# Performance work log

Measured on AMD Instinct MI355X. Metric: run time of the kernel, lower is better.

The kernel has to match this reference:

```python
import jax, jax.numpy as jnp
import numpy as np

B, L, V, OOV, E, H = 16, 256, 50000, 100, 128, 128
PAD_IDX, PLACEHOLDER_IDX = 0, 1


def lstm(x, W_ih, W_hh, b):
    # x: (B, T, I) -> hidden states (B, T, H); PyTorch gate order i,f,g,o
    nh = W_hh.shape[1]
    xg = jnp.einsum('bti,gi->btg', x, W_ih) + b  # precompute input gates

    def step(carry, xt):
        h, c = carry
        g = xt + h @ W_hh.T
        i, f, gg, o = jnp.split(g, 4, axis=-1)
        c = jax.nn.sigmoid(f) * c + jax.nn.sigmoid(i) * jnp.tanh(gg)
        h = jax.nn.sigmoid(o) * jnp.tanh(c)
        return (h, c), h

    bsz = x.shape[0]
    init = (jnp.zeros((bsz, nh), x.dtype), jnp.zeros((bsz, nh), x.dtype))
    _, hs = jax.lax.scan(step, init, jnp.swapaxes(xg, 0, 1))
    return jnp.swapaxes(hs, 0, 1)


def setup_inputs() -> dict:
    key = jax.random.key(0)
    ks = jax.random.split(key, 20)
    s = 0.05
    return {
        'src_tokens': jax.random.randint(ks[0], (B, L), 2, V),
        'src_lens': jnp.full((B,), L, dtype=jnp.int64 if jax.config.jax_enable_x64 else jnp.int32),
        'prev_output_tokens': jax.random.randint(ks[1], (B, 1), 2, V),
        'prev_output_lens': jnp.ones((B,), jnp.int32),
        'src_tokens_with_oov': jax.random.randint(ks[2], (B, L), 2, V + OOV),
        'oov_counts': jax.random.randint(ks[3], (B,), 0, OOV + 1),
        'decoder_state': jax.random.normal(ks[4], (B, H), jnp.float32),
        'embedding': jax.random.normal(ks[5], (V, E), jnp.float32) * 0.02,
        'enc_W_ih': jax.random.normal(ks[6], (4 * H, E), jnp.float32) * s,
        'enc_W_hh': jax.random.normal(ks[7], (4 * H, H), jnp.float32) * s,
        'enc_b': jnp.zeros((4 * H,), jnp.float32),
        'dec_W_ih': jax.random.normal(ks[8], (4 * H, E + H), jnp.float32) * s,
        'dec_W_hh': jax.random.normal(ks[9], (4 * H, H), jnp.float32) * s,
        'dec_b': jnp.zeros((4 * H,), jnp.float32),
        'attn_W': jax.random.normal(ks[10], (H, H), jnp.float32) * s,
        'out_W': jax.random.normal(ks[11], (H, 2 * H), jnp.float32) * s,
        'out_b': jnp.zeros((H,), jnp.float32),
        'copy_W': jax.random.normal(ks[12], (H, H), jnp.float32) * s,
        'gen_W': jax.random.normal(ks[13], (V + OOV, H), jnp.float32) * 0.02,
    }


def reference(src_tokens, src_lens, prev_output_tokens, prev_output_lens,
              src_tokens_with_oov, oov_counts, decoder_state,
              embedding, enc_W_ih, enc_W_hh, enc_b,
              dec_W_ih, dec_W_hh, dec_b,
              attn_W, out_W, out_b, copy_W, gen_W):
    neg_inf = -jnp.inf
    # ---- encoder ----
    enc_out = lstm(embedding[src_tokens], enc_W_ih, enc_W_hh, enc_b)  # B,L,H
    pad_mask = src_tokens == PAD_IDX                                   # B,L

    # ---- copy-state attention (selective read) ----
    mask = (prev_output_tokens == src_tokens).astype(enc_out.dtype)[..., None]  # B,L,1
    agg_w = jnp.tanh(jnp.einsum('blh,gh->blg', mask * enc_out, copy_W))
    cw = jax.nn.softmax(jnp.einsum('blg,bg->bl', agg_w, decoder_state), axis=1)
    copy_state = jnp.einsum('bl,blh->bh', cw, enc_out)

    # ---- decoder LSTM single step ----
    src_embed = embedding[prev_output_tokens[:, 0]]                    # B,E
    dec_in = jnp.concatenate([src_embed, copy_state], -1)[:, None, :]
    rnn_out = lstm(dec_in, dec_W_ih, dec_W_hh, dec_b)[:, 0]           # B,H

    # ---- attention ----
    scores = jnp.einsum('bh,blh->bl', rnn_out @ attn_W.T, enc_out)
    scores = jnp.where(pad_mask, neg_inf, scores)
    aw = jax.nn.softmax(scores, axis=1)
    ctx = jnp.einsum('bl,blh->bh', aw, enc_out)
    attn_out = jnp.tanh(jnp.concatenate([rnn_out, ctx], -1) @ out_W.T + out_b)

    # ---- generate + copy logits ----
    gen_logits = attn_out @ gen_W.T                                    # B,V+OOV
    b_idx = jnp.broadcast_to(jnp.arange(B)[:, None], (B, L))
    # scatter-reduce: equivalent to dense src_map (B, V+OOV, L) @ enc_out
    agg = jnp.zeros((B, V + OOV, H), enc_out.dtype).at[b_idx, src_tokens_with_oov].add(enc_out)
    copy_wts = jnp.tanh(jnp.einsum('bvh,gh->bvg', agg, copy_W))
    copy_score = jnp.einsum('bvg,bg->bv', copy_wts, attn_out)
    pos = jnp.arange(V + OOV)[None]
    copy_score = jnp.where(pos >= V + oov_counts[:, None], neg_inf, copy_score)

    total = gen_logits + copy_score
    total = jnp.where(pos == PLACEHOLDER_IDX, neg_inf, total)
    total_prob = jax.nn.softmax(total, axis=1)
    return total_prob, enc_out, attn_out
```

## Files before the change

kernel.cpp:

```cpp
#include <hip/hip_runtime.h>
#include <math.h>

#define B_   16
#define L_   256
#define V_   50000
#define NV_  50100
#define E_   128
#define H_   128
#define G4_  512
#define CHUNK_ 1566

typedef float f32x4 __attribute__((ext_vector_type(4)));
typedef float f32x2 __attribute__((ext_vector_type(2)));

__device__ __forceinline__ float sigm(float x){ return 1.0f/(1.0f+__expf(-x)); }
__device__ __forceinline__ float tanh_fast(float x){
  x = fminf(15.0f, fmaxf(-15.0f, x));
  float t = __expf(2.0f*x);
  return (t-1.0f)/(t+1.0f);
}

__global__ __launch_bounds__(512) void enc_xg_kernel(
    const int* __restrict__ tok, const float* __restrict__ emb,
    const float* __restrict__ Wih, const float* __restrict__ bias,
    float* __restrict__ xg)
{
  __shared__ __align__(16) float sx[8*128];
  int r0 = blockIdx.x*8;
  int t = threadIdx.x;
  for (int i=t; i<8*128; i+=512){
    int r=i>>7, e=i&127;
    sx[i] = emb[(size_t)tok[r0+r]*E_ + e];
  }
  __syncthreads();
  int g = t;
  float acc[8];
  #pragma unroll
  for (int r=0;r<8;r++) acc[r]=0.f;
  const float4* wr = (const float4*)(Wih + (size_t)g*E_);
  #pragma unroll 4
  for (int i=0;i<32;i++){
    float4 w = wr[i];
    #pragma unroll
    for (int r=0;r<8;r++){
      float4 x = ((const float4*)(sx + r*128))[i];
      acc[r] += w.x*x.x + w.y*x.y + w.z*x.z + w.w*x.w;
    }
  }
  float bg = bias[g];
  #pragma unroll
  for (int r=0;r<8;r++) xg[(size_t)(r0+r)*G4_ + g] = acc[r] + bg;
}

__global__ __launch_bounds__(512, 2) void enc_lstm_kernel(
    const float* __restrict__ xg, const float* __restrict__ Whh,
    float* __restrict__ enc_out)
{
  int b = blockIdx.x;
  int g = threadIdx.x;
  f32x2 w2[64];
  {
    const f32x4* wr4 = (const f32x4*)(Whh + (size_t)g*H_);
    #pragma unroll
    for (int k=0;k<32;k++){
      f32x4 wv = wr4[k];
      w2[2*k]   = wv.xy;
      w2[2*k+1] = wv.zw;
    }
  }

  __shared__ __align__(16) float sh_h[128];
  __shared__ float sh_g[512];
  if (g<128) sh_h[g]=0.f;
  float c = 0.f;
  const float* xgb = xg + (size_t)b*L_*G4_;
  float* eob = enc_out + (size_t)b*L_*H_;
  __syncthreads();

  const f32x4* sh4 = (const f32x4*)sh_h;
  bool is_gg = (g>=256 && g<384);
  float xcur = xgb[g];
  for (int t=0;t<L_;t++){
    float xnext = (t<L_-1) ? xgb[(t+1)*G4_ + g] : 0.f;
    f32x2 a0 = {xcur, 0.f}, a1 = {0.f,0.f}, a2 = {0.f,0.f}, a3 = {0.f,0.f};
    #pragma unroll
    for (int k=0;k<32;k+=4){
      f32x4 h0=sh4[k], h1=sh4[k+1], h2v=sh4[k+2], h3=sh4[k+3];
      a0 += w2[2*k+0]*h0.xy;  a1 += w2[2*k+1]*h0.zw;
      a2 += w2[2*k+2]*h1.xy;  a3 += w2[2*k+3]*h1.zw;
      a0 += w2[2*k+4]*h2v.xy; a1 += w2[2*k+5]*h2v.zw;
      a2 += w2[2*k+6]*h3.xy;  a3 += w2[2*k+7]*h3.zw;
    }
    f32x2 as = (a0+a1)+(a2+a3);
    float acc = as.x + as.y;
    float act = is_gg ? tanh_fast(acc) : sigm(acc);
    sh_g[g] = act;
    __syncthreads();
    if (g < 128){
      c = sh_g[128+g]*c + sh_g[g]*sh_g[256+g];
      float h = sh_g[384+g]*tanh_fast(c);
      sh_h[g] = h;
      eob[t*H_ + g] = h;
    }
    __syncthreads();
    xcur = xnext;
  }
}

__global__ __launch_bounds__(128) void copy_score1_kernel(
    const int* __restrict__ src, const int* __restrict__ prev,
    const float* __restrict__ enc_out, const float* __restrict__ cW,
    const float* __restrict__ dstate, float* __restrict__ s)
{
  int bl = blockIdx.x; int b = bl>>8;
  if (src[bl] != prev[b]){ if (threadIdx.x==0) s[bl]=0.f; return; }
  __shared__ __align__(16) float se[128];
  __shared__ float sred[2];
  int g = threadIdx.x;
  se[g] = enc_out[(size_t)bl*H_ + g];
  __syncthreads();
  const float4* wr = (const float4*)(cW + (size_t)g*H_);
  float acc=0.f;
  #pragma unroll
  for (int i=0;i<32;i++){
    float4 wv=wr[i]; float4 e=((const float4*)se)[i];
    acc += wv.x*e.x + wv.y*e.y + wv.z*e.z + wv.w*e.w;
  }
  float v = tanhf(acc)*dstate[b*H_+g];
  #pragma unroll
  for (int o=32;o;o>>=1) v += __shfl_down(v,o);
  if ((g&63)==0) sred[g>>6]=v;
  __syncthreads();
  if (g==0) s[bl]=sred[0]+sred[1];
}

__global__ __launch_bounds__(512) void fuse_mid_kernel(
    const float* __restrict__ scopy, const float* __restrict__ enc_out,
    const int* __restrict__ prev, const float* __restrict__ emb,
    const float* __restrict__ dWih, const float* __restrict__ db,
    const int* __restrict__ src, const float* __restrict__ aW,
    const float* __restrict__ oW, const float* __restrict__ ob,
    float* __restrict__ attn_out)
{
  int b=blockIdx.x, t=threadIdx.x;
  __shared__ float sw[256];
  __shared__ float spart[512];
  __shared__ float sred[4];
  __shared__ __align__(16) float sin_[256];
  __shared__ float sg[512];
  __shared__ __align__(16) float sr[128];
  __shared__ __align__(16) float sq[128];
  __shared__ float sc[256];
  __shared__ __align__(16) float sctx[128];

  float v = (t<256) ? scopy[b*L_+t] : -INFINITY;
  {
    float m=v;
    #pragma unroll
    for (int o=32;o;o>>=1) m=fmaxf(m,__shfl_down(m,o));
    if (t<256 && (t&63)==0) sred[t>>6]=m;
  }
  __syncthreads();
  float m4 = fmaxf(fmaxf(sred[0],sred[1]),fmaxf(sred[2],sred[3]));
  __syncthreads();
  float e = (t<256) ? __expf(v-m4) : 0.f;
  {
    float z=e;
    #pragma unroll
    for (int o=32;o;o>>=1) z += __shfl_down(z,o);
    if (t<256 && (t&63)==0) sred[t>>6]=z;
  }
  __syncthreads();
  {
    float z4 = sred[0]+sred[1]+sred[2]+sred[3];
    if (t<256) sw[t] = e/z4;
  }
  __syncthreads();

  {
    int ch=t>>7, h=t&127;
    float acc=0.f;
    const float* eb = enc_out + (size_t)b*L_*H_;
    for (int l=ch*64; l<ch*64+64; l++) acc += sw[l]*eb[(size_t)l*H_+h];
    spart[t]=acc;
  }
  __syncthreads();
  if (t<128){
    float cst = spart[t]+spart[128+t]+spart[256+t]+spart[384+t];
    sin_[128+t]=cst;
    sin_[t]=emb[(size_t)prev[b]*E_+t];
  }
  __syncthreads();

  {
    const f32x4* wr=(const f32x4*)(dWih + (size_t)t*256);
    const f32x4* x4=(const f32x4*)sin_;
    f32x2 d0={db[t],0.f}, d1={0.f,0.f}, d2={0.f,0.f}, d3={0.f,0.f};
    #pragma unroll
    for (int k=0;k<64;k+=4){
      f32x4 xa=x4[k], xb=x4[k+1], xc=x4[k+2], xd=x4[k+3];
      f32x4 wa=wr[k], wb=wr[k+1], wc=wr[k+2], wd=wr[k+3];
      d0 += wa.xy*xa.xy; d1 += wa.zw*xa.zw;
      d2 += wb.xy*xb.xy; d3 += wb.zw*xb.zw;
      d0 += wc.xy*xc.xy; d1 += wc.zw*xc.zw;
      d2 += wd.xy*xd.xy; d3 += wd.zw*xd.zw;
    }
    f32x2 dsm=(d0+d1)+(d2+d3);
    sg[t]=dsm.x+dsm.y;
  }
  __syncthreads();
  if (t<128){
    float iv=sg[t], gv=sg[256+t], ov=sg[384+t];
    float cc = sigm(iv)*tanhf(gv);
    sr[t] = sigm(ov)*tanhf(cc);
  }
  __syncthreads();

  if (t<128){
    const f32x4* wr=(const f32x4*)(aW + (size_t)t*H_);
    const f32x4* x4=(const f32x4*)sr;
    float acc=0.f;
    #pragma unroll
    for (int i=0;i<32;i++){
      f32x4 wv=wr[i], x=x4[i];
      acc += wv.x*x.x + wv.y*x.y + wv.z*x.z + wv.w*x.w;
    }
    sq[t]=acc;
  }
  __syncthreads();

  if (t<256){
    const f32x4* e4=(const f32x4*)(enc_out + ((size_t)b*L_+t)*H_);
    const f32x4* q4=(const f32x4*)sq;
    float acc=0.f;
    #pragma unroll
    for (int i=0;i<32;i++){
      f32x4 ev=e4[i], q=q4[i];
      acc += ev.x*q.x + ev.y*q.y + ev.z*q.z + ev.w*q.w;
    }
    if (src[b*L_+t]==0) acc=-INFINITY;
    sc[t]=acc;
  }
  __syncthreads();

  v = (t<256) ? sc[t] : -INFINITY;
  {
    float m=v;
    #pragma unroll
    for (int o=32;o;o>>=1) m=fmaxf(m,__shfl_down(m,o));
    if (t<256 && (t&63)==0) sred[t>>6]=m;
  }
  __syncthreads();
  m4 = fmaxf(fmaxf(sred[0],sred[1]),fmaxf(sred[2],sred[3]));
  __syncthreads();
  e = (t<256) ? __expf(v-m4) : 0.f;
  {
    float z=e;
    #pragma unroll
    for (int o=32;o;o>>=1) z += __shfl_down(z,o);
    if (t<256 && (t&63)==0) sred[t>>6]=z;
  }
  __syncthreads();
  {
    float z4 = sred[0]+sred[1]+sred[2]+sred[3];
    if (t<256) sc[t] = e/z4;
  }
  __syncthreads();

  {
    int ch=t>>7, h=t&127;
    float acc=0.f;
    const float* eb = enc_out + (size_t)b*L_*H_;
    for (int l=ch*64; l<ch*64+64; l++) acc += sc[l]*eb[(size_t)l*H_+h];
    spart[t]=acc;
  }
  __syncthreads();
  if (t<128) sctx[t] = spart[t]+spart[128+t]+spart[256+t]+spart[384+t];
  __syncthreads();

  if (t<128){
    const f32x4* wr=(const f32x4*)(oW + (size_t)t*256);
    const f32x4* r4=(const f32x4*)sr;
    const f32x4* c4=(const f32x4*)sctx;
    float acc=ob[t];
    #pragma unroll
    for (int i=0;i<32;i++){
      f32x4 wv=wr[i], x=r4[i];
      acc += wv.x*x.x + wv.y*x.y + wv.z*x.z + wv.w*x.w;
    }
    #pragma unroll
    for (int i=0;i<32;i++){
      f32x4 wv=wr[32+i], x=c4[i];
      acc += wv.x*x.x + wv.y*x.y + wv.z*x.z + wv.w*x.w;
    }
    attn_out[b*H_+t]=tanhf(acc);
  }
}

__global__ __launch_bounds__(256) void copy_agg_kernel(
    const int* __restrict__ stw, const float* __restrict__ enc_out,
    float* __restrict__ agg, int* __restrict__ replist, int* __restrict__ repcnt)
{
  int b=blockIdx.x, l=threadIdx.x;
  __shared__ int stok[256];
  __shared__ int scnt;
  stok[l] = stw[b*L_+l];
  if (l==0) scnt=0;
  __syncthreads();
  int tok = stok[l];
  int first=0;
  while (stok[first]!=tok) first++;
  if (first==l){
    int myidx = atomicAdd(&scnt,1);
    float4 acc[32];
    #pragma unroll
    for (int i=0;i<32;i++) acc[i]=make_float4(0.f,0.f,0.f,0.f);
    for (int l2=l; l2<L_; l2++){
      if (stok[l2]==tok){
        const float4* e=(const float4*)(enc_out + ((size_t)b*L_+l2)*H_);
        #pragma unroll
        for (int i=0;i<32;i++){
          float4 v=e[i];
          acc[i].x+=v.x; acc[i].y+=v.y; acc[i].z+=v.z; acc[i].w+=v.w;
        }
      }
    }
    float4* dst=(float4*)(agg + ((size_t)b*L_+l)*H_);
    #pragma unroll
    for (int i=0;i<32;i++) dst[i]=acc[i];
    replist[b*L_+myidx]=l;
  }
  __syncthreads();
  if (l==0) repcnt[b]=scnt;
}

__global__ __launch_bounds__(256) void gen_logits_kernel(
    const float* __restrict__ attn_out, const float* __restrict__ gW,
    const int* __restrict__ oovc, float* __restrict__ total)
{
  __shared__ float sa[B_*H_];
  __shared__ float sw[64*129];
  int t=threadIdx.x;
  int v0=blockIdx.x*64;
  for (int i=t;i<B_*H_;i+=256) sa[i]=attn_out[i];
  for (int i=t;i<64*32;i+=256){
    int r=i>>5, cc=i&31;
    if (v0+r<NV_){
      float4 wv = ((const float4*)(gW + (size_t)(v0+r)*H_))[cc];
      float* dst = sw + r*129 + cc*4;
      dst[0]=wv.x; dst[1]=wv.y; dst[2]=wv.z; dst[3]=wv.w;
    }
  }
  __syncthreads();
  int vl=t&63, bq=t>>6;
  int v=v0+vl;
  if (v>=NV_) return;
  float acc[4]={0.f,0.f,0.f,0.f};
  const float* wrow = sw + vl*129;
  #pragma unroll 8
  for (int h4=0; h4<32; h4++){
    float w0=wrow[h4*4+0], w1=wrow[h4*4+1], w2=wrow[h4*4+2], w3=wrow[h4*4+3];
    #pragma unroll
    for (int k=0;k<4;k++){
      float4 a = ((const float4*)(sa + (bq*4+k)*H_))[h4];
      acc[k] += w0*a.x + w1*a.y + w2*a.z + w3*a.w;
    }
  }
  #pragma unroll
  for (int k=0;k<4;k++){
    int b=bq*4+k;
    float o = (v==1 || v >= V_ + oovc[b]) ? -INFINITY : acc[k];
    total[(size_t)b*NV_ + v] = o;
  }
}

__global__ __launch_bounds__(128) void copy_score2_kernel(
    const int* __restrict__ stw, const float* __restrict__ agg,
    const float* __restrict__ cW, const float* __restrict__ attn_out,
    const int* __restrict__ replist, const int* __restrict__ repcnt,
    float* __restrict__ total)
{
  int b=blockIdx.x;
  int cnt=repcnt[b];
  int g=threadIdx.x;
  __shared__ __align__(16) float srow[128];
  __shared__ float sred[2];
  float aog = attn_out[b*H_+g];
  float4 w[32];
  const float4* wrow=(const float4*)(cW + (size_t)g*H_);
  #pragma unroll
  for (int i=0;i<32;i++) w[i]=wrow[i];
  for (int ri=blockIdx.y; ri<cnt; ri+=gridDim.y){
    int l = replist[b*L_+ri];
    srow[g] = agg[((size_t)b*L_+l)*H_+g];
    __syncthreads();
    float acc=0.f;
    #pragma unroll
    for (int i=0;i<32;i++){
      float4 e=((const float4*)srow)[i]; float4 wv=w[i];
      acc += wv.x*e.x + wv.y*e.y + wv.z*e.z + wv.w*e.w;
    }
    float v = tanhf(acc)*aog;
    #pragma unroll
    for (int o=32;o;o>>=1) v += __shfl_down(v,o);
    if ((g&63)==0) sred[g>>6]=v;
    __syncthreads();
    if (g==0){
      int vtok = stw[b*L_+l];
      total[(size_t)b*NV_ + vtok] += sred[0]+sred[1];
    }
    __syncthreads();
  }
}

__global__ __launch_bounds__(256) void vocab_pass1_kernel(
    const float* __restrict__ total, float* __restrict__ pmax, float* __restrict__ psum)
{
  int b=blockIdx.x, j=blockIdx.y, t=threadIdx.x;
  int lo=j*CHUNK_, hi=min(lo+CHUNK_, NV_);
  const float* row = total + (size_t)b*NV_;
  __shared__ float sred[4];
  float m=-INFINITY;
  for (int i=lo+t;i<hi;i+=256) m=fmaxf(m,row[i]);
  #pragma unroll
  for (int o=32;o;o>>=1) m=fmaxf(m,__shfl_down(m,o));
  if ((t&63)==0) sred[t>>6]=m;
  __syncthreads();
  m = fmaxf(fmaxf(sred[0],sred[1]),fmaxf(sred[2],sred[3]));
  __syncthreads();
  float s=0.f;
  if (m > -INFINITY){
    for (int i=lo+t;i<hi;i+=256) s += __expf(row[i]-m);
    #pragma unroll
    for (int o=32;o;o>>=1) s += __shfl_down(s,o);
  }
  if ((t&63)==0) sred[t>>6]=s;
  __syncthreads();
  if (t==0){ pmax[b*32+j]=m; psum[b*32+j]=sred[0]+sred[1]+sred[2]+sred[3]; }
}

__global__ void vocab_pass2_kernel(const float* __restrict__ pmax,
                                   const float* __restrict__ psum, float* __restrict__ MZ)
{
  int b=blockIdx.x, t=threadIdx.x;
  float mj = pmax[b*32+t];
  float m = mj;
  #pragma unroll
  for (int o=16;o;o>>=1) m=fmaxf(m,__shfl_down(m,o));
  m = __shfl(m,0);
  float z = psum[b*32+t]*__expf(mj-m);
  #pragma unroll
  for (int o=16;o;o>>=1) z += __shfl_down(z,o);
  if (t==0){ MZ[b]=m; MZ[16+b]=z; }
}

__global__ __launch_bounds__(256) void vocab_pass3_kernel(
    float* __restrict__ total, const float* __restrict__ MZ)
{
  int b=blockIdx.x, j=blockIdx.y, t=threadIdx.x;
  int lo=j*CHUNK_, hi=min(lo+CHUNK_, NV_);
  float m=MZ[b], rz=1.0f/MZ[16+b];
  float* row = total + (size_t)b*NV_;
  for (int i=lo+t;i<hi;i+=256) row[i] = __expf(row[i]-m)*rz;
}

extern "C" void kernel_launch(void* const* d_in, const int* in_sizes, int n_in,
                              void* d_out, int out_size, void* d_ws, size_t ws_size,
                              hipStream_t stream)
{
  const int*   src_tokens = (const int*)d_in[0];
  const int*   prev_tok   = (const int*)d_in[2];
  const int*   stw        = (const int*)d_in[4];
  const int*   oovc       = (const int*)d_in[5];
  const float* dstate     = (const float*)d_in[6];
  const float* emb        = (const float*)d_in[7];
  const float* enc_Wih    = (const float*)d_in[8];
  const float* enc_Whh    = (const float*)d_in[9];
  const float* enc_b      = (const float*)d_in[10];
  const float* dec_Wih    = (const float*)d_in[11];
  const float* dec_b      = (const float*)d_in[13];
  const float* attn_W     = (const float*)d_in[14];
  const float* out_W      = (const float*)d_in[15];
  const float* out_b      = (const float*)d_in[16];
  const float* copy_W     = (const float*)d_in[17];
  const float* gen_W      = (const float*)d_in[18];

  float* out      = (float*)d_out;
  float* total    = out;
  float* enc_out  = out + (size_t)B_*NV_;
  float* attn_out = enc_out + (size_t)B_*L_*H_;

  float* ws     = (float*)d_ws;
  float* xg     = ws;
  float* agg    = xg + (size_t)B_*L_*G4_;
  float* scopy  = agg + (size_t)B_*L_*H_;
  float* pmax   = scopy + B_*L_;
  float* psum   = pmax + 512;
  float* MZ     = psum + 512;
  int*   replist= (int*)(MZ + 32);
  int*   repcnt = replist + B_*L_;

  enc_xg_kernel<<<B_*L_/8, 512, 0, stream>>>(src_tokens, emb, enc_Wih, enc_b, xg);
  enc_lstm_kernel<<<B_, 512, 0, stream>>>(xg, enc_Whh, enc_out);
  copy_score1_kernel<<<B_*L_, 128, 0, stream>>>(src_tokens, prev_tok, enc_out, copy_W, dstate, scopy);
  copy_agg_kernel<<<B_, 256, 0, stream>>>(stw, enc_out, agg, replist, repcnt);
  fuse_mid_kernel<<<B_, 512, 0, stream>>>(scopy, enc_out, prev_tok, emb, dec_Wih, dec_b,
                                          src_tokens, attn_W, out_W, out_b, attn_out);
  gen_logits_kernel<<<(NV_+63)/64, 256, 0, stream>>>(attn_out, gen_W, oovc, total);
  copy_score2_kernel<<<dim3(B_,32), 128, 0, stream>>>(stw, agg, copy_W, attn_out, replist, repcnt, total);
  vocab_pass1_kernel<<<dim3(B_,32), 256, 0, stream>>>(total, pmax, psum);
  vocab_pass2_kernel<<<B_, 32, 0, stream>>>(pmax, psum, MZ);
  vocab_pass3_kernel<<<dim3(B_,32), 256, 0, stream>>>(total, MZ);
}
```

Baseline: 340.8 us.

## Fuse copy-score into mid kernel, merge vocab reductions, retile encoder input GEMM

```diff
diff --git a/kernel.cpp b/kernel.cpp
--- a/kernel.cpp
+++ b/kernel.cpp
@@ -25,34 +25,35 @@
     const float* __restrict__ Wih, const float* __restrict__ bias,
     float* __restrict__ xg)
 {
-  __shared__ __align__(16) float sx[8*128];
-  int r0 = blockIdx.x*8;
+  __shared__ __align__(16) float sx[16*128];
+  int r0 = blockIdx.x*16;
   int t = threadIdx.x;
-  for (int i=t; i<8*128; i+=512){
+  for (int i=t; i<16*128; i+=512){
     int r=i>>7, e=i&127;
     sx[i] = emb[(size_t)tok[r0+r]*E_ + e];
   }
   __syncthreads();
   int g = t;
-  float acc[8];
-  #pragma unroll
-  for (int r=0;r<8;r++) acc[r]=0.f;
-  const float4* wr = (const float4*)(Wih + (size_t)g*E_);
-  #pragma unroll 4
+  float acc[16];
+  #pragma unroll
+  for (int r=0;r<16;r++) acc[r]=0.f;
+  const f32x4* wr = (const f32x4*)(Wih + (size_t)g*E_);
+  #pragma unroll 2
   for (int i=0;i<32;i++){
-    float4 w = wr[i];
-    #pragma unroll
-    for (int r=0;r<8;r++){
-      float4 x = ((const float4*)(sx + r*128))[i];
+    f32x4 w = wr[i];
+    #pragma unroll
+    for (int r=0;r<16;r++){
+      f32x4 x = ((const f32x4*)(sx + r*128))[i];
       acc[r] += w.x*x.x + w.y*x.y + w.z*x.z + w.w*x.w;
     }
   }
   float bg = bias[g];
   #pragma unroll
-  for (int r=0;r<8;r++) xg[(size_t)(r0+r)*G4_ + g] = acc[r] + bg;
-}
-
-__global__ __launch_bounds__(512, 2) void enc_lstm_kernel(
+  for (int r=0;r<16;r++) xg[(size_t)(r0+r)*G4_ + g] = acc[r] + bg;
+}
+
+__global__ void __attribute__((amdgpu_flat_work_group_size(512,512), amdgpu_waves_per_eu(2,2)))
+enc_lstm_kernel(
     const float* __restrict__ xg, const float* __restrict__ Whh,
     float* __restrict__ enc_out)
 {
@@ -68,6 +69,8 @@
       w2[2*k+1] = wv.zw;
     }
   }
+  #pragma unroll
+  for (int k=0;k<64;k++) asm volatile("" : "+v"(w2[k]));
 
   __shared__ __align__(16) float sh_h[128];
   __shared__ float sh_g[512];
@@ -107,42 +110,19 @@
   }
 }
 
-__global__ __launch_bounds__(128) void copy_score1_kernel(
+__global__ __launch_bounds__(512) void fuse_mid_kernel(
     const int* __restrict__ src, const int* __restrict__ prev,
     const float* __restrict__ enc_out, const float* __restrict__ cW,
-    const float* __restrict__ dstate, float* __restrict__ s)
-{
-  int bl = blockIdx.x; int b = bl>>8;
-  if (src[bl] != prev[b]){ if (threadIdx.x==0) s[bl]=0.f; return; }
+    const float* __restrict__ dstate, const float* __restrict__ emb,
+    const float* __restrict__ dWih, const float* __restrict__ db,
+    const float* __restrict__ aW, const float* __restrict__ oW,
+    const float* __restrict__ ob, float* __restrict__ attn_out)
+{
+  int b=blockIdx.x, t=threadIdx.x;
+  __shared__ float s_scopy[256];
+  __shared__ int   mlist[256];
+  __shared__ int   mcnt;
   __shared__ __align__(16) float se[128];
-  __shared__ float sred[2];
-  int g = threadIdx.x;
-  se[g] = enc_out[(size_t)bl*H_ + g];
-  __syncthreads();
-  const float4* wr = (const float4*)(cW + (size_t)g*H_);
-  float acc=0.f;
-  #pragma unroll
-  for (int i=0;i<32;i++){
-    float4 wv=wr[i]; float4 e=((const float4*)se)[i];
-    acc += wv.x*e.x + wv.y*e.y + wv.z*e.z + wv.w*e.w;
-  }
-  float v = tanhf(acc)*dstate[b*H_+g];
-  #pragma unroll
-  for (int o=32;o;o>>=1) v += __shfl_down(v,o);
-  if ((g&63)==0) sred[g>>6]=v;
-  __syncthreads();
-  if (g==0) s[bl]=sred[0]+sred[1];
-}
-
-__global__ __launch_bounds__(512) void fuse_mid_kernel(
-    const float* __restrict__ scopy, const float* __restrict__ enc_out,
-    const int* __restrict__ prev, const float* __restrict__ emb,
-    const float* __restrict__ dWih, const float* __restrict__ db,
-    const int* __restrict__ src, const float* __restrict__ aW,
-    const float* __restrict__ oW, const float* __restrict__ ob,
-    float* __restrict__ attn_out)
-{
-  int b=blockIdx.x, t=threadIdx.x;
   __shared__ float sw[256];
   __shared__ float spart[512];
   __shared__ float sred[4];
@@ -153,7 +133,37 @@
   __shared__ float sc[256];
   __shared__ __align__(16) float sctx[128];
 
-  float v = (t<256) ? scopy[b*L_+t] : -INFINITY;
+  if (t==0) mcnt=0;
+  __syncthreads();
+  if (t<256){
+    s_scopy[t]=0.f;
+    if (src[b*L_+t]==prev[b]){ int i=atomicAdd(&mcnt,1); mlist[i]=t; }
+  }
+  __syncthreads();
+  for (int mi=0; mi<mcnt; mi++){
+    int l = mlist[mi];
+    if (t<128) se[t] = enc_out[((size_t)b*L_+l)*H_ + t];
+    __syncthreads();
+    if (t<128){
+      const f32x4* wr = (const f32x4*)(cW + (size_t)t*H_);
+      const f32x4* e4 = (const f32x4*)se;
+      float acc=0.f;
+      #pragma unroll
+      for (int i=0;i<32;i++){
+        f32x4 wv=wr[i], e=e4[i];
+        acc += wv.x*e.x + wv.y*e.y + wv.z*e.z + wv.w*e.w;
+      }
+      float v = tanhf(acc)*dstate[b*H_+t];
+      #pragma unroll
+      for (int o=32;o;o>>=1) v += __shfl_down(v,o);
+      if ((t&63)==0) sred[t>>6]=v;
+    }
+    __syncthreads();
+    if (t==0) s_scopy[l]=sred[0]+sred[1];
+    __syncthreads();
+  }
+
+  float v = (t<256) ? s_scopy[t] : -INFINITY;
   {
     float m=v;
     #pragma unroll
@@ -312,20 +322,17 @@
   while (stok[first]!=tok) first++;
   if (first==l){
     int myidx = atomicAdd(&scnt,1);
-    float4 acc[32];
-    #pragma unroll
-    for (int i=0;i<32;i++) acc[i]=make_float4(0.f,0.f,0.f,0.f);
+    f32x4 acc[32];
+    #pragma unroll
+    for (int i=0;i<32;i++) acc[i]=(f32x4){0.f,0.f,0.f,0.f};
     for (int l2=l; l2<L_; l2++){
       if (stok[l2]==tok){
-        const float4* e=(const float4*)(enc_out + ((size_t)b*L_+l2)*H_);
+        const f32x4* e=(const f32x4*)(enc_out + ((size_t)b*L_+l2)*H_);
         #pragma unroll
-        for (int i=0;i<32;i++){
-          float4 v=e[i];
-          acc[i].x+=v.x; acc[i].y+=v.y; acc[i].z+=v.z; acc[i].w+=v.w;
-        }
+        for (int i=0;i<32;i++) acc[i]+=e[i];
       }
     }
-    float4* dst=(float4*)(agg + ((size_t)b*L_+l)*H_);
+    f32x4* dst=(f32x4*)(agg + ((size_t)b*L_+l)*H_);
     #pragma unroll
     for (int i=0;i<32;i++) dst[i]=acc[i];
     replist[b*L_+myidx]=l;
@@ -386,8 +393,8 @@
   __shared__ __align__(16) float srow[128];
   __shared__ float sred[2];
   float aog = attn_out[b*H_+g];
-  float4 w[32];
-  const float4* wrow=(const float4*)(cW + (size_t)g*H_);
+  f32x4 w[32];
+  const f32x4* wrow=(const f32x4*)(cW + (size_t)g*H_);
   #pragma unroll
   for (int i=0;i<32;i++) w[i]=wrow[i];
   for (int ri=blockIdx.y; ri<cnt; ri+=gridDim.y){
@@ -397,7 +404,7 @@
     float acc=0.f;
     #pragma unroll
     for (int i=0;i<32;i++){
-      float4 e=((const float4*)srow)[i]; float4 wv=w[i];
+      f32x4 e=((const f32x4*)srow)[i]; f32x4 wv=w[i];
       acc += wv.x*e.x + wv.y*e.y + wv.z*e.z + wv.w*e.w;
     }
     float v = tanhf(acc)*aog;
@@ -413,48 +420,42 @@
   }
 }
 
-__global__ __launch_bounds__(256) void vocab_pass1_kernel(
-    const float* __restrict__ total, float* __restrict__ pmax, float* __restrict__ psum)
-{
-  int b=blockIdx.x, j=blockIdx.y, t=threadIdx.x;
-  int lo=j*CHUNK_, hi=min(lo+CHUNK_, NV_);
+__global__ __launch_bounds__(1024) void vocab_reduce_kernel(
+    const float* __restrict__ total, float* __restrict__ MZ)
+{
+  int b=blockIdx.x, t=threadIdx.x;
   const float* row = total + (size_t)b*NV_;
-  __shared__ float sred[4];
+  __shared__ float sred[16];
   float m=-INFINITY;
-  for (int i=lo+t;i<hi;i+=256) m=fmaxf(m,row[i]);
+  for (int i=t;i<NV_;i+=1024) m=fmaxf(m,row[i]);
   #pragma unroll
   for (int o=32;o;o>>=1) m=fmaxf(m,__shfl_down(m,o));
   if ((t&63)==0) sred[t>>6]=m;
   __syncthreads();
-  m = fmaxf(fmaxf(sred[0],sred[1]),fmaxf(sred[2],sred[3]));
-  __syncthreads();
+  if (t<64){
+    float mm = (t<16) ? sred[t] : -INFINITY;
+    #pragma unroll
+    for (int o=8;o;o>>=1) mm=fmaxf(mm,__shfl_down(mm,o));
+    if (t==0) sred[0]=mm;
+  }
+  __syncthreads();
+  m = sred[0];
   float s=0.f;
-  if (m > -INFINITY){
-    for (int i=lo+t;i<hi;i+=256) s += __expf(row[i]-m);
-    #pragma unroll
-    for (int o=32;o;o>>=1) s += __shfl_down(s,o);
-  }
+  for (int i=t;i<NV_;i+=1024) s += __expf(row[i]-m);
+  #pragma unroll
+  for (int o=32;o;o>>=1) s += __shfl_down(s,o);
+  __syncthreads();
   if ((t&63)==0) sred[t>>6]=s;
   __syncthreads();
-  if (t==0){ pmax[b*32+j]=m; psum[b*32+j]=sred[0]+sred[1]+sred[2]+sred[3]; }
-}
-
-__global__ void vocab_pass2_kernel(const float* __restrict__ pmax,
-                                   const float* __restrict__ psum, float* __restrict__ MZ)
-{
-  int b=blockIdx.x, t=threadIdx.x;
-  float mj = pmax[b*32+t];
-  float m = mj;
-  #pragma unroll
-  for (int o=16;o;o>>=1) m=fmaxf(m,__shfl_down(m,o));
-  m = __shfl(m,0);
-  float z = psum[b*32+t]*__expf(mj-m);
-  #pragma unroll
-  for (int o=16;o;o>>=1) z += __shfl_down(z,o);
-  if (t==0){ MZ[b]=m; MZ[16+b]=z; }
-}
-
-__global__ __launch_bounds__(256) void vocab_pass3_kernel(
+  if (t<64){
+    float ss = (t<16) ? sred[t] : 0.f;
+    #pragma unroll
+    for (int o=8;o;o>>=1) ss += __shfl_down(ss,o);
+    if (t==0){ MZ[b]=m; MZ[16+b]=ss; }
+  }
+}
+
+__global__ __launch_bounds__(256) void vocab_norm_kernel(
     float* __restrict__ total, const float* __restrict__ MZ)
 {
   int b=blockIdx.x, j=blockIdx.y, t=threadIdx.x;
@@ -493,22 +494,17 @@
   float* ws     = (float*)d_ws;
   float* xg     = ws;
   float* agg    = xg + (size_t)B_*L_*G4_;
-  float* scopy  = agg + (size_t)B_*L_*H_;
-  float* pmax   = scopy + B_*L_;
-  float* psum   = pmax + 512;
-  float* MZ     = psum + 512;
+  float* MZ     = agg + (size_t)B_*L_*H_;
   int*   replist= (int*)(MZ + 32);
   int*   repcnt = replist + B_*L_;
 
-  enc_xg_kernel<<<B_*L_/8, 512, 0, stream>>>(src_tokens, emb, enc_Wih, enc_b, xg);
+  enc_xg_kernel<<<B_*L_/16, 512, 0, stream>>>(src_tokens, emb, enc_Wih, enc_b, xg);
   enc_lstm_kernel<<<B_, 512, 0, stream>>>(xg, enc_Whh, enc_out);
-  copy_score1_kernel<<<B_*L_, 128, 0, stream>>>(src_tokens, prev_tok, enc_out, copy_W, dstate, scopy);
+  fuse_mid_kernel<<<B_, 512, 0, stream>>>(src_tokens, prev_tok, enc_out, copy_W, dstate,
+                                          emb, dec_Wih, dec_b, attn_W, out_W, out_b, attn_out);
   copy_agg_kernel<<<B_, 256, 0, stream>>>(stw, enc_out, agg, replist, repcnt);
-  fuse_mid_kernel<<<B_, 512, 0, stream>>>(scopy, enc_out, prev_tok, emb, dec_Wih, dec_b,
-                                          src_tokens, attn_W, out_W, out_b, attn_out);
   gen_logits_kernel<<<(NV_+63)/64, 256, 0, stream>>>(attn_out, gen_W, oovc, total);
   copy_score2_kernel<<<dim3(B_,32), 128, 0, stream>>>(stw, agg, copy_W, attn_out, replist, repcnt, total);
-  vocab_pass1_kernel<<<dim3(B_,32), 256, 0, stream>>>(total, pmax, psum);
-  vocab_pass2_kernel<<<B_, 32, 0, stream>>>(pmax, psum, MZ);
-  vocab_pass3_kernel<<<dim3(B_,32), 256, 0, stream>>>(total, MZ);
-}
+  vocab_reduce_kernel<<<B_, 1024, 0, stream>>>(total, MZ);
+  vocab_norm_kernel<<<dim3(B_,32), 256, 0, stream>>>(total, MZ);
+}
```

Result: slower. 350.6 us (+2.9%).
